# Performance work log

Hardware: AMD Instinct MI355X
Metric: run time of the kernel (lower is better)

The kernel has to match this reference:

```python
import jax, jax.numpy as jnp
import numpy as np

# Dopri5 Butcher tableau (6 effective stages; 5th-order weights, b7 = 0)
_AT = np.zeros((6, 6), dtype=np.float64)
_AT[1, :1] = [1/5]
_AT[2, :2] = [3/40, 9/40]
_AT[3, :3] = [44/45, -56/15, 32/9]
_AT[4, :4] = [19372/6561, -25360/2187, 64448/6561, -212/729]
_AT[5, :5] = [9017/3168, -355/33, 46732/5247, 49/176, -5103/18656]
_BT = np.array([35/384, 0.0, 500/1113, 125/192, -2187/6784, 11/84], dtype=np.float64)
_CT = np.array([0.0, 1/5, 3/10, 4/5, 8/9, 1.0], dtype=np.float64)


def _spline_derivs(u, dt):
    # diffrax backward_hermite_coefficients: backward-difference derivatives,
    # first point copies the second. u: (B, T, m)
    d = (u[:, 1:] - u[:, :-1]) / dt
    return jnp.concatenate([d[:, :1], d], axis=1)


def _hermite(u0, u1, d0, d1, dt, s):
    # cubic Hermite on normalized coordinate s in [0, 1]
    s2 = s * s
    s3 = s2 * s
    return ((2 * s3 - 3 * s2 + 1) * u0 + ((s3 - 2 * s2 + s) * dt) * d0
            + (-2 * s3 + 3 * s2) * u1 + ((s3 - s2) * dt) * d1)


def _flow(t, u, x0, A, Bm, b, C):
    dt = t[1] - t[0]  # ConstantStepSize with dt0 = t[1] (t[0] == 0)
    du = _spline_derivs(u, dt)

    def vf(x, uu):  # system.vector_field
        return jnp.tanh(x @ A + uu @ Bm + b)

    # per-interval spline data, time-major for scan: each (T-1, B, m)
    seq = tuple(jnp.swapaxes(a, 0, 1)
                for a in (u[:, :-1], u[:, 1:], du[:, :-1], du[:, 1:]))

    def step(x, inp):
        u0, u1, d0, d1 = inp
        ks = []
        for j in range(6):
            xj = x
            for i in range(j):
                aji = float(_AT[j, i])
                if aji != 0.0:
                    xj = xj + (dt * aji) * ks[i]
            uj = _hermite(u0, u1, d0, d1, dt, float(_CT[j]))
            ks.append(vf(xj, uj))
        x_new = x + dt * sum(float(_BT[j]) * ks[j]
                             for j in range(6) if float(_BT[j]) != 0.0)
        return x_new, x_new

    _, xs = jax.lax.scan(step, x0, seq)               # (T-1, B, d)
    x_traj = jnp.concatenate([x0[None], xs], axis=0)  # (T, B, d)
    x_traj = jnp.swapaxes(x_traj, 0, 1)               # (B, T, d)
    y = x_traj @ C                                    # system.output, (B, T, p)
    return x_traj, y


def setup_inputs() -> dict:
    key = jax.random.key(0)
    ks = jax.random.split(key, 6)
    B, T, d, m, p = 64, 1024, 256, 128, 64
    dt = 0.01
    t = jnp.arange(T, dtype=jnp.float32) * dt
    u = jax.random.normal(ks[0], (B, T, m), dtype=jnp.float32)
    x0 = jax.random.normal(ks[1], (B, d), dtype=jnp.float32)
    A = jax.random.normal(ks[2], (d, d), dtype=jnp.float32) / np.float32(np.sqrt(d))
    Bm = jax.random.normal(ks[3], (m, d), dtype=jnp.float32) / np.float32(np.sqrt(m))
    b = jax.random.normal(ks[4], (d,), dtype=jnp.float32) * 0.1
    C = jax.random.normal(ks[5], (d, p), dtype=jnp.float32) / np.float32(np.sqrt(d))
    return {"t": t, "u": u, "x0": x0, "A": A, "Bm": Bm, "b": b, "C": C}


def reference(t, u, x0, A, Bm, b, C):
    return _flow(t, u, x0, A, Bm, b, C)
```

## Files before the change

### kernel.cpp

```cpp
#include <hip/hip_runtime.h>

typedef unsigned short ushort_t;
typedef unsigned int uint_t;
typedef __attribute__((ext_vector_type(8))) short bf16x8;
typedef __attribute__((ext_vector_type(4))) float f32x4;

#define Tn 1024
#define Dd 256
#define Mm 128
#define Pp 64

__device__ __forceinline__ float bf2f(ushort_t s) {
    union { uint_t u; float f; } c; c.u = ((uint_t)s) << 16; return c.f;
}
__device__ __forceinline__ ushort_t f2bf(float f) {
    union { float f; uint_t u; } c; c.f = f;
    uint_t u = c.u;
    return (ushort_t)((u + 0x7fffu + ((u >> 16) & 1u)) >> 16);
}
__device__ __forceinline__ float bflo(uint_t w) {
    union { uint_t u; float f; } c; c.u = w << 16; return c.f;
}
__device__ __forceinline__ float bfhi(uint_t w) {
    union { uint_t u; float f; } c; c.u = w & 0xffff0000u; return c.f;
}
__device__ __forceinline__ void dot2(float& acc, uint_t a, uint_t b) {
    asm("v_dot2_f32_bf16 %0, %1, %2, %0" : "+v"(acc) : "v"(a), "v"(b));
}
__device__ __forceinline__ void split3(float v, ushort_t& h, ushort_t& m, ushort_t& l) {
    h = f2bf(v);
    float r1 = v - bf2f(h);
    m = f2bf(r1);
    float r2 = r1 - bf2f(m);
    l = f2bf(r2);
}

template <bool BF16>
__device__ __forceinline__ float ldin(const void* p, size_t i) {
    if constexpr (BF16) return bf2f(((const ushort_t*)p)[i]);
    else return ((const float*)p)[i];
}
template <bool BF16>
__device__ __forceinline__ void stout(void* p, size_t i, float v) {
    if constexpr (BF16) ((ushort_t*)p)[i] = f2bf(v);
    else ((float*)p)[i] = v;
}
template <bool BF16>
__device__ __forceinline__ uint_t pack2(const void* p, size_t i0, size_t i1) {
    return (uint_t)f2bf(ldin<BF16>(p, i0)) | ((uint_t)f2bf(ldin<BF16>(p, i1)) << 16);
}

template <bool BF16>
__global__ __launch_bounds__(512, 1)
void flow_kernel(const void* __restrict__ tg, const void* __restrict__ ug,
                 const void* __restrict__ x0g, const void* __restrict__ Ag,
                 const void* __restrict__ Bg, const void* __restrict__ bg,
                 const void* __restrict__ Cg, void* __restrict__ outv) {
    const bool is_bf16 = (((const uint_t*)tg)[0] != 0u);
    if (is_bf16 != BF16) return;

    __shared__ __align__(16) uint_t ringhi[4 * 64];
    __shared__ __align__(16) uint_t ujh[4 * 64], ujm[4 * 64], ujl[4 * 64];
    __shared__ __align__(16) uint_t xh[2][128], xm[2][128], xl[2][128];
    __shared__ __align__(16) uint_t zbuf[128];

    const int tid = threadIdx.x;
    const int b = blockIdx.x;
    const int lane = tid & 63;
    const int w = tid >> 6;
    const int colj = lane & 15;
    const int rowg = lane >> 4;
    const int j1 = w * 32 + colj;
    const int j2 = j1 + 16;

    const int c = tid & 7;
    const int g = tid >> 3;
    const int p = g;
    int rx[4];
#pragma unroll
    for (int q = 0; q < 4; ++q) rx[q] = (q + c) & 3;

    const float dtf = ldin<BF16>(tg, 1) - ldin<BF16>(tg, 0);
    const size_t ub = (size_t)b * Tn * Mm;
    const size_t ybase = (size_t)gridDim.x * Tn * Dd;

    bf16x8 Wf0[8], Wf1[8], Bf0[4], Bf1[4];
#pragma unroll
    for (int ks = 0; ks < 8; ++ks) {
        const int k0 = ks * 32 + rowg * 8;
        uint4 u0, u1;
        u0.x = pack2<BF16>(Ag, (size_t)(k0 + 0) * Dd + j1, (size_t)(k0 + 1) * Dd + j1);
        u0.y = pack2<BF16>(Ag, (size_t)(k0 + 2) * Dd + j1, (size_t)(k0 + 3) * Dd + j1);
        u0.z = pack2<BF16>(Ag, (size_t)(k0 + 4) * Dd + j1, (size_t)(k0 + 5) * Dd + j1);
        u0.w = pack2<BF16>(Ag, (size_t)(k0 + 6) * Dd + j1, (size_t)(k0 + 7) * Dd + j1);
        u1.x = pack2<BF16>(Ag, (size_t)(k0 + 0) * Dd + j2, (size_t)(k0 + 1) * Dd + j2);
        u1.y = pack2<BF16>(Ag, (size_t)(k0 + 2) * Dd + j2, (size_t)(k0 + 3) * Dd + j2);
        u1.z = pack2<BF16>(Ag, (size_t)(k0 + 4) * Dd + j2, (size_t)(k0 + 5) * Dd + j2);
        u1.w = pack2<BF16>(Ag, (size_t)(k0 + 6) * Dd + j2, (size_t)(k0 + 7) * Dd + j2);
        Wf0[ks] = __builtin_bit_cast(bf16x8, u0);
        Wf1[ks] = __builtin_bit_cast(bf16x8, u1);
    }
#pragma unroll
    for (int ks = 0; ks < 4; ++ks) {
        const int k0 = ks * 32 + rowg * 8;
        uint4 u0, u1;
        u0.x = pack2<BF16>(Bg, (size_t)(k0 + 0) * Dd + j1, (size_t)(k0 + 1) * Dd + j1);
        u0.y = pack2<BF16>(Bg, (size_t)(k0 + 2) * Dd + j1, (size_t)(k0 + 3) * Dd + j1);
        u0.z = pack2<BF16>(Bg, (size_t)(k0 + 4) * Dd + j1, (size_t)(k0 + 5) * Dd + j1);
        u0.w = pack2<BF16>(Bg, (size_t)(k0 + 6) * Dd + j1, (size_t)(k0 + 7) * Dd + j1);
        u1.x = pack2<BF16>(Bg, (size_t)(k0 + 0) * Dd + j2, (size_t)(k0 + 1) * Dd + j2);
        u1.y = pack2<BF16>(Bg, (size_t)(k0 + 2) * Dd + j2, (size_t)(k0 + 3) * Dd + j2);
        u1.z = pack2<BF16>(Bg, (size_t)(k0 + 4) * Dd + j2, (size_t)(k0 + 5) * Dd + j2);
        u1.w = pack2<BF16>(Bg, (size_t)(k0 + 6) * Dd + j2, (size_t)(k0 + 7) * Dd + j2);
        Bf0[ks] = __builtin_bit_cast(bf16x8, u0);
        Bf1[ks] = __builtin_bit_cast(bf16x8, u1);
    }
    uint_t Cpack[16];
#pragma unroll
    for (int q = 0; q < 4; ++q) {
        const int kc = c * 32 + rx[q] * 8;
#pragma unroll
        for (int ww = 0; ww < 4; ++ww)
            Cpack[q * 4 + ww] = pack2<BF16>(Cg, (size_t)(kc + 2 * ww) * Pp + p,
                                            (size_t)(kc + 2 * ww + 1) * Pp + p);
    }
    const float bj1 = ldin<BF16>(bg, j1);
    const float bj2 = ldin<BF16>(bg, j2);

    float x1 = ldin<BF16>(x0g, (size_t)b * Dd + j1);
    float x2 = ldin<BF16>(x0g, (size_t)b * Dd + j2);
    if (tid < 128) {
        float e0 = ldin<BF16>(x0g, (size_t)b * Dd + 2 * tid);
        float e1 = ldin<BF16>(x0g, (size_t)b * Dd + 2 * tid + 1);
        ushort_t h0, m0, l0, h1, m1, l1;
        split3(e0, h0, m0, l0);
        split3(e1, h1, m1, l1);
        xh[0][tid] = (uint_t)h0 | ((uint_t)h1 << 16);
        xm[0][tid] = (uint_t)m0 | ((uint_t)m1 << 16);
        xl[0][tid] = (uint_t)l0 | ((uint_t)l1 << 16);
        zbuf[tid] = 0u;
    }
    if (rowg == 0) {
        stout<BF16>(outv, (size_t)b * Tn * Dd + j1, x1);
        stout<BF16>(outv, (size_t)b * Tn * Dd + j2, x2);
    }
    if (tid < 64) {
#pragma unroll
        for (int row = 0; row < 3; ++row) {
            uint_t wv;
            if constexpr (BF16) {
                wv = ((const uint_t*)ug)[((ub + (size_t)row * Mm) >> 1) + tid];
            } else {
                wv = pack2<BF16>(ug, ub + (size_t)row * Mm + 2 * tid,
                                 ub + (size_t)row * Mm + 2 * tid + 1);
            }
            ringhi[row * 64 + tid] = wv;
        }
    }
    __syncthreads();

    {
        const uint4* ph = (const uint4*)xh[0] + c * 4;
        const uint4* pm = (const uint4*)xm[0] + c * 4;
        const uint4* pl = (const uint4*)xl[0] + c * 4;
        float ah = 0.f, am = 0.f, al = 0.f;
#pragma unroll
        for (int q = 0; q < 4; ++q) {
            uint4 vh = ph[rx[q]];
            uint4 vm = pm[rx[q]];
            uint4 vl = pl[rx[q]];
            dot2(ah, vh.x, Cpack[q * 4 + 0]); dot2(ah, vh.y, Cpack[q * 4 + 1]);
            dot2(ah, vh.z, Cpack[q * 4 + 2]); dot2(ah, vh.w, Cpack[q * 4 + 3]);
            dot2(am, vm.x, Cpack[q * 4 + 0]); dot2(am, vm.y, Cpack[q * 4 + 1]);
            dot2(am, vm.z, Cpack[q * 4 + 2]); dot2(am, vm.w, Cpack[q * 4 + 3]);
            dot2(al, vl.x, Cpack[q * 4 + 0]); dot2(al, vl.y, Cpack[q * 4 + 1]);
            dot2(al, vl.z, Cpack[q * 4 + 2]); dot2(al, vl.w, Cpack[q * 4 + 3]);
        }
        float ay = (ah + am) + al;
        ay += __shfl_xor(ay, 1, 64);
        ay += __shfl_xor(ay, 2, 64);
        ay += __shfl_xor(ay, 4, 64);
        if (c == 0) stout<BF16>(outv, ybase + (size_t)b * Tn * Pp + p, ay);
    }

    constexpr float ATc[6][5] = {
        {0.f, 0.f, 0.f, 0.f, 0.f},
        {0.2f, 0.f, 0.f, 0.f, 0.f},
        {0.075f, 0.225f, 0.f, 0.f, 0.f},
        {(float)(44.0 / 45.0), (float)(-56.0 / 15.0), (float)(32.0 / 9.0), 0.f, 0.f},
        {(float)(19372.0 / 6561.0), (float)(-25360.0 / 2187.0), (float)(64448.0 / 6561.0),
         (float)(-212.0 / 729.0), 0.f},
        {(float)(9017.0 / 3168.0), (float)(-355.0 / 33.0), (float)(46732.0 / 5247.0),
         (float)(49.0 / 176.0), (float)(-5103.0 / 18656.0)}};
    constexpr float BTc[6] = {(float)(35.0 / 384.0), 0.f, (float)(500.0 / 1113.0),
                              (float)(125.0 / 192.0), (float)(-2187.0 / 6784.0),
                              (float)(11.0 / 84.0)};

    float k1r[6], k2r[6];

    for (int n = 0; n < Tn - 1; ++n) {
        uint_t preg = 0;
        if (tid < 64 && n + 3 < Tn) {
            if constexpr (BF16)
                preg = ((const uint_t*)ug)[((ub + (size_t)(n + 3) * Mm) >> 1) + tid];
            else
                preg = pack2<BF16>(ug, ub + (size_t)(n + 3) * Mm + 2 * tid,
                                   ub + (size_t)(n + 3) * Mm + 2 * tid + 1);
        }

#pragma unroll
        for (int s = 0; s < 6; ++s) {
            const int src = s & 1;
            const uint4* xb = (const uint4*)(colj < 4 ? xh[src] : colj < 8 ? xm[src]
                                             : colj < 12 ? xl[src] : zbuf);
            const uint4* ub4;
            if (s == 0 || s == 5) {
                const uint4* rb = (const uint4*)(ringhi + (((s == 0) ? n : n + 1) & 3) * 64);
                ub4 = (colj < 4) ? rb : (const uint4*)zbuf;
            } else {
                const uint4* uh = (const uint4*)ujh + (s - 1) * 16;
                const uint4* um = (const uint4*)ujm + (s - 1) * 16;
                const uint4* ul = (const uint4*)ujl + (s - 1) * 16;
                ub4 = colj < 4 ? uh : colj < 8 ? um : colj < 12 ? ul : (const uint4*)zbuf;
            }
            f32x4 ax_a = {0.f, 0.f, 0.f, 0.f}, ax_b = {0.f, 0.f, 0.f, 0.f};
            f32x4 ay_a = {0.f, 0.f, 0.f, 0.f}, ay_b = {0.f, 0.f, 0.f, 0.f};
            f32x4 au_1 = {0.f, 0.f, 0.f, 0.f}, au_2 = {0.f, 0.f, 0.f, 0.f};
#pragma unroll
            for (int ks = 0; ks < 4; ++ks) {
                bf16x8 xf = __builtin_bit_cast(bf16x8, xb[ks * 4 + rowg]);
                ax_a = __builtin_amdgcn_mfma_f32_16x16x32_bf16(xf, Wf0[ks], ax_a, 0, 0, 0);
                ay_a = __builtin_amdgcn_mfma_f32_16x16x32_bf16(xf, Wf1[ks], ay_a, 0, 0, 0);
            }
#pragma unroll
            for (int ks = 4; ks < 8; ++ks) {
                bf16x8 xf = __builtin_bit_cast(bf16x8, xb[ks * 4 + rowg]);
                ax_b = __builtin_amdgcn_mfma_f32_16x16x32_bf16(xf, Wf0[ks], ax_b, 0, 0, 0);
                ay_b = __builtin_amdgcn_mfma_f32_16x16x32_bf16(xf, Wf1[ks], ay_b, 0, 0, 0);
            }
#pragma unroll
            for (int ks = 0; ks < 4; ++ks) {
                bf16x8 uf = __builtin_bit_cast(bf16x8, ub4[ks * 4 + rowg]);
                au_1 = __builtin_amdgcn_mfma_f32_16x16x32_bf16(uf, Bf0[ks], au_1, 0, 0, 0);
                au_2 = __builtin_amdgcn_mfma_f32_16x16x32_bf16(uf, Bf1[ks], au_2, 0, 0, 0);
            }
            float s1v = (ax_a[0] + ax_b[0]) + au_1[0];
            float s2v = (ay_a[0] + ay_b[0]) + au_2[0];
            float t1 = s1v + __shfl_xor(s1v, 16, 64);
            float t2 = s2v + __shfl_xor(s2v, 16, 64);
            float z1 = t1 + __shfl_xor(t1, 32, 64) + bj1;
            float z2 = t2 + __shfl_xor(t2, 32, 64) + bj2;
            float e1v = __expf(2.f * z1);
            float d1v = e1v + 1.f;
            float r1 = __builtin_amdgcn_rcpf(d1v);
            r1 = r1 * fmaf(-d1v, r1, 2.f);
            k1r[s] = fmaf(-2.f, r1, 1.f);
            float e2v = __expf(2.f * z2);
            float d2v = e2v + 1.f;
            float r2 = __builtin_amdgcn_rcpf(d2v);
            r2 = r2 * fmaf(-d2v, r2, 2.f);
            k2r[s] = fmaf(-2.f, r2, 1.f);

            float pv1, pv2;
            if (s < 5) {
                pv1 = x1; pv2 = x2;
#pragma unroll
                for (int i2 = 0; i2 <= s; ++i2) {
                    pv1 = fmaf(dtf * ATc[s + 1][i2], k1r[i2], pv1);
                    pv2 = fmaf(dtf * ATc[s + 1][i2], k2r[i2], pv2);
                }
            } else {
#pragma unroll
                for (int i2 = 0; i2 < 6; ++i2)
                    if (BTc[i2] != 0.f) {
                        x1 = fmaf(dtf * BTc[i2], k1r[i2], x1);
                        x2 = fmaf(dtf * BTc[i2], k2r[i2], x2);
                    }
                pv1 = x1; pv2 = x2;
            }
            if (rowg == 0) {
                const int dst = (s + 1) & 1;
                ushort_t h1, m1, l1, h2, m2, l2;
                split3(pv1, h1, m1, l1);
                split3(pv2, h2, m2, l2);
                ushort_t* ph = (ushort_t*)xh[dst];
                ushort_t* pm = (ushort_t*)xm[dst];
                ushort_t* pl = (ushort_t*)xl[dst];
                ph[j1] = h1; pm[j1] = m1; pl[j1] = l1;
                ph[j2] = h2; pm[j2] = m2; pl[j2] = l2;
            }
            if (s == 0) {
                if (tid < 256) {
                    const int st = tid >> 6, q2 = tid & 63;
                    uint_t u0w = ringhi[((n) & 3) * 64 + q2];
                    uint_t u1w = ringhi[((n + 1) & 3) * 64 + q2];
                    uint_t umw = ringhi[((n - 1) & 3) * 64 + q2];
                    float u0a = bflo(u0w), u0b = bfhi(u0w);
                    float u1a = bflo(u1w), u1b = bfhi(u1w);
                    float uma = bflo(umw), umb = bfhi(umw);
                    float dca = u1a - u0a, dcb = u1b - u0b;
                    float dpa = (n == 0) ? dca : (u0a - uma);
                    float dpb = (n == 0) ? dcb : (u0b - umb);
                    float HA = st == 0 ? 0.896f : st == 1 ? 0.784f : st == 2 ? 0.104f : (float)(25.0 / 729.0);
                    float HB = st == 0 ? 0.128f : st == 1 ? 0.147f : st == 2 ? 0.032f : (float)(8.0 / 729.0);
                    float HG = st == 0 ? 0.104f : st == 1 ? 0.216f : st == 2 ? 0.896f : (float)(704.0 / 729.0);
                    float HD = st == 0 ? -0.032f : st == 1 ? -0.063f : st == 2 ? -0.128f : (float)(-64.0 / 729.0);
                    float ja = HA * u0a + HG * u1a + HB * dpa + HD * dca;
                    float jb = HA * u0b + HG * u1b + HB * dpb + HD * dcb;
                    ushort_t ha, ma, la, hb, mb, lb;
                    split3(ja, ha, ma, la);
                    split3(jb, hb, mb, lb);
                    ujh[st * 64 + q2] = (uint_t)ha | ((uint_t)hb << 16);
                    ujm[st * 64 + q2] = (uint_t)ma | ((uint_t)mb << 16);
                    ujl[st * 64 + q2] = (uint_t)la | ((uint_t)lb << 16);
                }
            }
            __syncthreads();
        }

        {
            const uint4* ph = (const uint4*)xh[0] + c * 4;
            const uint4* pm = (const uint4*)xm[0] + c * 4;
            const uint4* pl = (const uint4*)xl[0] + c * 4;
            float ah = 0.f, am = 0.f, al = 0.f;
#pragma unroll
            for (int q = 0; q < 4; ++q) {
                uint4 vh = ph[rx[q]];
                uint4 vm = pm[rx[q]];
                uint4 vl = pl[rx[q]];
                dot2(ah, vh.x, Cpack[q * 4 + 0]); dot2(ah, vh.y, Cpack[q * 4 + 1]);
                dot2(ah, vh.z, Cpack[q * 4 + 2]); dot2(ah, vh.w, Cpack[q * 4 + 3]);
                dot2(am, vm.x, Cpack[q * 4 + 0]); dot2(am, vm.y, Cpack[q * 4 + 1]);
                dot2(am, vm.z, Cpack[q * 4 + 2]); dot2(am, vm.w, Cpack[q * 4 + 3]);
                dot2(al, vl.x, Cpack[q * 4 + 0]); dot2(al, vl.y, Cpack[q * 4 + 1]);
                dot2(al, vl.z, Cpack[q * 4 + 2]); dot2(al, vl.w, Cpack[q * 4 + 3]);
            }
            float ay = (ah + am) + al;
            ay += __shfl_xor(ay, 1, 64);
            ay += __shfl_xor(ay, 2, 64);
            ay += __shfl_xor(ay, 4, 64);
            if (c == 0)
                stout<BF16>(outv, ybase + (size_t)b * Tn * Pp + (size_t)(n + 1) * Pp + p, ay);
        }
        if (rowg == 0) {
            stout<BF16>(outv, (size_t)b * Tn * Dd + (size_t)(n + 1) * Dd + j1, x1);
            stout<BF16>(outv, (size_t)b * Tn * Dd + (size_t)(n + 1) * Dd + j2, x2);
        }
        if (tid < 64 && n + 3 < Tn) ringhi[((n + 3) & 3) * 64 + tid] = preg;
    }
}

extern "C" void kernel_launch(void* const* d_in, const int* in_sizes, int n_in,
                              void* d_out, int out_size, void* d_ws, size_t ws_size,
                              hipStream_t stream) {
    const void* t  = d_in[0];
    const void* u  = d_in[1];
    const void* x0 = d_in[2];
    const void* A  = d_in[3];
    const void* Bm = d_in[4];
    const void* bb = d_in[5];
    const void* C  = d_in[6];

    const int B = in_sizes[2] / Dd;

    flow_kernel<true><<<dim3(B), dim3(512), 0, stream>>>(t, u, x0, A, Bm, bb, C, d_out);
    flow_kernel<false><<<dim3(B), dim3(512), 0, stream>>>(t, u, x0, A, Bm, bb, C, d_out);
}
```

Before: 5.458 ms.

## Remap hi/mid/lo splits to MFMA rows and pad a unified LDS buffer

Puts the hi, mid and lo bf16 components of the state and input vectors on MFMA A-operand rows 0-2, with the other rows zeroed, instead of spreading them across column groups. The three parts can then be summed inside each lane's accumulator registers, which removes the cross-lane xor shuffles from every RK stage. Only lanes 0-15 now do the tanh and stage update. All shared arrays are merged into one padded LDS buffer to cut bank conflicts, and only the lanes that need operand data read from LDS. The aim is to shorten the serial per-stage critical path; the cost is a more intricate index mapping that must match the MFMA output layout.

```diff
diff --git a/kernel.cpp b/kernel.cpp
--- a/kernel.cpp
+++ b/kernel.cpp
@@ -9,6 +9,18 @@
 #define Dd 256
 #define Mm 128
 #define Pp 64
+
+#define XH0 0
+#define XH1 128
+#define XM0 260
+#define XM1 388
+#define XL0 532
+#define XL1 660
+#define UJH 800
+#define UJM 1060
+#define UJL 1332
+#define RING 1600
+#define LDSW 1856
 
 __device__ __forceinline__ float bf2f(ushort_t s) {
     union { uint_t u; float f; } c; c.u = ((uint_t)s) << 16; return c.f;
@@ -59,10 +71,7 @@
     const bool is_bf16 = (((const uint_t*)tg)[0] != 0u);
     if (is_bf16 != BF16) return;
 
-    __shared__ __align__(16) uint_t ringhi[4 * 64];
-    __shared__ __align__(16) uint_t ujh[4 * 64], ujm[4 * 64], ujl[4 * 64];
-    __shared__ __align__(16) uint_t xh[2][128], xm[2][128], xl[2][128];
-    __shared__ __align__(16) uint_t zbuf[128];
+    __shared__ __align__(16) uint_t lds[LDSW];
 
     const int tid = threadIdx.x;
     const int b = blockIdx.x;
@@ -83,6 +92,10 @@
     const float dtf = ldin<BF16>(tg, 1) - ldin<BF16>(tg, 0);
     const size_t ub = (size_t)b * Tn * Mm;
     const size_t ybase = (size_t)gridDim.x * Tn * Dd;
+
+    const uint_t xbase0 = (colj == 0) ? XH0 : (colj == 1) ? XM0 : XL0;
+    const uint_t xbase1 = (colj == 0) ? XH1 : (colj == 1) ? XM1 : XL1;
+    const uint_t ujbase = (colj == 0) ? UJH : (colj == 1) ? UJM : UJL;
 
     bf16x8 Wf0[8], Wf1[8], Bf0[4], Bf1[4];
 #pragma unroll
@@ -135,12 +148,11 @@
         ushort_t h0, m0, l0, h1, m1, l1;
         split3(e0, h0, m0, l0);
         split3(e1, h1, m1, l1);
-        xh[0][tid] = (uint_t)h0 | ((uint_t)h1 << 16);
-        xm[0][tid] = (uint_t)m0 | ((uint_t)m1 << 16);
-        xl[0][tid] = (uint_t)l0 | ((uint_t)l1 << 16);
-        zbuf[tid] = 0u;
-    }
-    if (rowg == 0) {
+        lds[XH0 + tid] = (uint_t)h0 | ((uint_t)h1 << 16);
+        lds[XM0 + tid] = (uint_t)m0 | ((uint_t)m1 << 16);
+        lds[XL0 + tid] = (uint_t)l0 | ((uint_t)l1 << 16);
+    }
+    if (lane < 16) {
         stout<BF16>(outv, (size_t)b * Tn * Dd + j1, x1);
         stout<BF16>(outv, (size_t)b * Tn * Dd + j2, x2);
     }
@@ -154,15 +166,15 @@
                 wv = pack2<BF16>(ug, ub + (size_t)row * Mm + 2 * tid,
                                  ub + (size_t)row * Mm + 2 * tid + 1);
             }
-            ringhi[row * 64 + tid] = wv;
+            lds[RING + row * 64 + tid] = wv;
         }
     }
     __syncthreads();
 
     {
-        const uint4* ph = (const uint4*)xh[0] + c * 4;
-        const uint4* pm = (const uint4*)xm[0] + c * 4;
-        const uint4* pl = (const uint4*)xl[0] + c * 4;
+        const uint4* ph = (const uint4*)(lds + XH0) + c * 4;
+        const uint4* pm = (const uint4*)(lds + XM0) + c * 4;
+        const uint4* pl = (const uint4*)(lds + XL0) + c * 4;
         float ah = 0.f, am = 0.f, al = 0.f;
 #pragma unroll
         for (int q = 0; q < 4; ++q) {
@@ -210,91 +222,98 @@
 
 #pragma unroll
         for (int s = 0; s < 6; ++s) {
-            const int src = s & 1;
-            const uint4* xb = (const uint4*)(colj < 4 ? xh[src] : colj < 8 ? xm[src]
-                                             : colj < 12 ? xl[src] : zbuf);
-            const uint4* ub4;
+            uint4 xfr[8] = {{0u,0u,0u,0u},{0u,0u,0u,0u},{0u,0u,0u,0u},{0u,0u,0u,0u},
+                            {0u,0u,0u,0u},{0u,0u,0u,0u},{0u,0u,0u,0u},{0u,0u,0u,0u}};
+            if (colj < 3) {
+                const uint4* xb = (const uint4*)(lds + ((s & 1) ? xbase1 : xbase0));
+#pragma unroll
+                for (int ks = 0; ks < 8; ++ks) xfr[ks] = xb[ks * 4 + rowg];
+            }
+            uint4 ufr[4] = {{0u,0u,0u,0u},{0u,0u,0u,0u},{0u,0u,0u,0u},{0u,0u,0u,0u}};
             if (s == 0 || s == 5) {
-                const uint4* rb = (const uint4*)(ringhi + (((s == 0) ? n : n + 1) & 3) * 64);
-                ub4 = (colj < 4) ? rb : (const uint4*)zbuf;
+                if (colj == 0) {
+                    const uint4* rb =
+                        (const uint4*)(lds + RING + (((s == 0) ? n : n + 1) & 3) * 64);
+#pragma unroll
+                    for (int ks = 0; ks < 4; ++ks) ufr[ks] = rb[ks * 4 + rowg];
+                }
             } else {
-                const uint4* uh = (const uint4*)ujh + (s - 1) * 16;
-                const uint4* um = (const uint4*)ujm + (s - 1) * 16;
-                const uint4* ul = (const uint4*)ujl + (s - 1) * 16;
-                ub4 = colj < 4 ? uh : colj < 8 ? um : colj < 12 ? ul : (const uint4*)zbuf;
+                if (colj < 3) {
+                    const uint4* ujb = (const uint4*)(lds + ujbase + (s - 1) * 64);
+#pragma unroll
+                    for (int ks = 0; ks < 4; ++ks) ufr[ks] = ujb[ks * 4 + rowg];
+                }
             }
             f32x4 ax_a = {0.f, 0.f, 0.f, 0.f}, ax_b = {0.f, 0.f, 0.f, 0.f};
             f32x4 ay_a = {0.f, 0.f, 0.f, 0.f}, ay_b = {0.f, 0.f, 0.f, 0.f};
             f32x4 au_1 = {0.f, 0.f, 0.f, 0.f}, au_2 = {0.f, 0.f, 0.f, 0.f};
 #pragma unroll
             for (int ks = 0; ks < 4; ++ks) {
-                bf16x8 xf = __builtin_bit_cast(bf16x8, xb[ks * 4 + rowg]);
+                bf16x8 xf = __builtin_bit_cast(bf16x8, xfr[ks]);
                 ax_a = __builtin_amdgcn_mfma_f32_16x16x32_bf16(xf, Wf0[ks], ax_a, 0, 0, 0);
                 ay_a = __builtin_amdgcn_mfma_f32_16x16x32_bf16(xf, Wf1[ks], ay_a, 0, 0, 0);
             }
 #pragma unroll
             for (int ks = 4; ks < 8; ++ks) {
-                bf16x8 xf = __builtin_bit_cast(bf16x8, xb[ks * 4 + rowg]);
+                bf16x8 xf = __builtin_bit_cast(bf16x8, xfr[ks]);
                 ax_b = __builtin_amdgcn_mfma_f32_16x16x32_bf16(xf, Wf0[ks], ax_b, 0, 0, 0);
                 ay_b = __builtin_amdgcn_mfma_f32_16x16x32_bf16(xf, Wf1[ks], ay_b, 0, 0, 0);
             }
 #pragma unroll
             for (int ks = 0; ks < 4; ++ks) {
-                bf16x8 uf = __builtin_bit_cast(bf16x8, ub4[ks * 4 + rowg]);
+                bf16x8 uf = __builtin_bit_cast(bf16x8, ufr[ks]);
                 au_1 = __builtin_amdgcn_mfma_f32_16x16x32_bf16(uf, Bf0[ks], au_1, 0, 0, 0);
                 au_2 = __builtin_amdgcn_mfma_f32_16x16x32_bf16(uf, Bf1[ks], au_2, 0, 0, 0);
             }
-            float s1v = (ax_a[0] + ax_b[0]) + au_1[0];
-            float s2v = (ay_a[0] + ay_b[0]) + au_2[0];
-            float t1 = s1v + __shfl_xor(s1v, 16, 64);
-            float t2 = s2v + __shfl_xor(s2v, 16, 64);
-            float z1 = t1 + __shfl_xor(t1, 32, 64) + bj1;
-            float z2 = t2 + __shfl_xor(t2, 32, 64) + bj2;
-            float e1v = __expf(2.f * z1);
-            float d1v = e1v + 1.f;
-            float r1 = __builtin_amdgcn_rcpf(d1v);
-            r1 = r1 * fmaf(-d1v, r1, 2.f);
-            k1r[s] = fmaf(-2.f, r1, 1.f);
-            float e2v = __expf(2.f * z2);
-            float d2v = e2v + 1.f;
-            float r2 = __builtin_amdgcn_rcpf(d2v);
-            r2 = r2 * fmaf(-d2v, r2, 2.f);
-            k2r[s] = fmaf(-2.f, r2, 1.f);
-
-            float pv1, pv2;
-            if (s < 5) {
-                pv1 = x1; pv2 = x2;
-#pragma unroll
-                for (int i2 = 0; i2 <= s; ++i2) {
-                    pv1 = fmaf(dtf * ATc[s + 1][i2], k1r[i2], pv1);
-                    pv2 = fmaf(dtf * ATc[s + 1][i2], k2r[i2], pv2);
+            if (lane < 16) {
+                float z1 = ((ax_a[0] + ax_a[1] + ax_a[2]) + (ax_b[0] + ax_b[1] + ax_b[2]))
+                         + (au_1[0] + au_1[1] + au_1[2]) + bj1;
+                float z2 = ((ay_a[0] + ay_a[1] + ay_a[2]) + (ay_b[0] + ay_b[1] + ay_b[2]))
+                         + (au_2[0] + au_2[1] + au_2[2]) + bj2;
+                float e1v = __expf(2.f * z1);
+                float d1v = e1v + 1.f;
+                float r1 = __builtin_amdgcn_rcpf(d1v);
+                r1 = r1 * fmaf(-d1v, r1, 2.f);
+                k1r[s] = fmaf(-2.f, r1, 1.f);
+                float e2v = __expf(2.f * z2);
+                float d2v = e2v + 1.f;
+                float r2 = __builtin_amdgcn_rcpf(d2v);
+                r2 = r2 * fmaf(-d2v, r2, 2.f);
+                k2r[s] = fmaf(-2.f, r2, 1.f);
+
+                float pv1, pv2;
+                if (s < 5) {
+                    pv1 = x1; pv2 = x2;
+#pragma unroll
+                    for (int i2 = 0; i2 <= s; ++i2) {
+                        pv1 = fmaf(dtf * ATc[s + 1][i2], k1r[i2], pv1);
+                        pv2 = fmaf(dtf * ATc[s + 1][i2], k2r[i2], pv2);
+                    }
+                } else {
+#pragma unroll
+                    for (int i2 = 0; i2 < 6; ++i2)
+                        if (BTc[i2] != 0.f) {
+                            x1 = fmaf(dtf * BTc[i2], k1r[i2], x1);
+                            x2 = fmaf(dtf * BTc[i2], k2r[i2], x2);
+                        }
+                    pv1 = x1; pv2 = x2;
                 }
-            } else {
-#pragma unroll
-                for (int i2 = 0; i2 < 6; ++i2)
-                    if (BTc[i2] != 0.f) {
-                        x1 = fmaf(dtf * BTc[i2], k1r[i2], x1);
-                        x2 = fmaf(dtf * BTc[i2], k2r[i2], x2);
-                    }
-                pv1 = x1; pv2 = x2;
-            }
-            if (rowg == 0) {
                 const int dst = (s + 1) & 1;
                 ushort_t h1, m1, l1, h2, m2, l2;
                 split3(pv1, h1, m1, l1);
                 split3(pv2, h2, m2, l2);
-                ushort_t* ph = (ushort_t*)xh[dst];
-                ushort_t* pm = (ushort_t*)xm[dst];
-                ushort_t* pl = (ushort_t*)xl[dst];
-                ph[j1] = h1; pm[j1] = m1; pl[j1] = l1;
-                ph[j2] = h2; pm[j2] = m2; pl[j2] = l2;
+                ushort_t* wh = (ushort_t*)(lds + (dst ? XH1 : XH0));
+                ushort_t* wm = (ushort_t*)(lds + (dst ? XM1 : XM0));
+                ushort_t* wl = (ushort_t*)(lds + (dst ? XL1 : XL0));
+                wh[j1] = h1; wm[j1] = m1; wl[j1] = l1;
+                wh[j2] = h2; wm[j2] = m2; wl[j2] = l2;
             }
             if (s == 0) {
                 if (tid < 256) {
                     const int st = tid >> 6, q2 = tid & 63;
-                    uint_t u0w = ringhi[((n) & 3) * 64 + q2];
-                    uint_t u1w = ringhi[((n + 1) & 3) * 64 + q2];
-                    uint_t umw = ringhi[((n - 1) & 3) * 64 + q2];
+                    uint_t u0w = lds[RING + ((n) & 3) * 64 + q2];
+                    uint_t u1w = lds[RING + ((n + 1) & 3) * 64 + q2];
+                    uint_t umw = lds[RING + ((n - 1) & 3) * 64 + q2];
                     float u0a = bflo(u0w), u0b = bfhi(u0w);
                     float u1a = bflo(u1w), u1b = bfhi(u1w);
                     float uma = bflo(umw), umb = bfhi(umw);
@@ -310,18 +329,18 @@
                     ushort_t ha, ma, la, hb, mb, lb;
                     split3(ja, ha, ma, la);
                     split3(jb, hb, mb, lb);
-                    ujh[st * 64 + q2] = (uint_t)ha | ((uint_t)hb << 16);
-                    ujm[st * 64 + q2] = (uint_t)ma | ((uint_t)mb << 16);
-                    ujl[st * 64 + q2] = (uint_t)la | ((uint_t)lb << 16);
+                    lds[UJH + st * 64 + q2] = (uint_t)ha | ((uint_t)hb << 16);
+                    lds[UJM + st * 64 + q2] = (uint_t)ma | ((uint_t)mb << 16);
+                    lds[UJL + st * 64 + q2] = (uint_t)la | ((uint_t)lb << 16);
                 }
             }
             __syncthreads();
         }
 
         {
-            const uint4* ph = (const uint4*)xh[0] + c * 4;
-            const uint4* pm = (const uint4*)xm[0] + c * 4;
-            const uint4* pl = (const uint4*)xl[0] + c * 4;
+            const uint4* ph = (const uint4*)(lds + XH0) + c * 4;
+            const uint4* pm = (const uint4*)(lds + XM0) + c * 4;
+            const uint4* pl = (const uint4*)(lds + XL0) + c * 4;
             float ah = 0.f, am = 0.f, al = 0.f;
 #pragma unroll
             for (int q = 0; q < 4; ++q) {
@@ -342,11 +361,11 @@
             if (c == 0)
                 stout<BF16>(outv, ybase + (size_t)b * Tn * Pp + (size_t)(n + 1) * Pp + p, ay);
         }
-        if (rowg == 0) {
+        if (lane < 16) {
             stout<BF16>(outv, (size_t)b * Tn * Dd + (size_t)(n + 1) * Dd + j1, x1);
             stout<BF16>(outv, (size_t)b * Tn * Dd + (size_t)(n + 1) * Dd + j2, x2);
         }
-        if (tid < 64 && n + 3 < Tn) ringhi[((n + 3) & 3) * 64 + tid] = preg;
+        if (tid < 64 && n + 3 < Tn) lds[RING + ((n + 3) & 3) * 64 + tid] = preg;
     }
 }
 
```

Result: slower. 5.959 ms (+9.2%).
